# Performance work log

Measured on AMD Instinct MI355X. Metric: run time of the kernel, lower is better.

## Reference

```python
import jax, jax.numpy as jnp
import numpy as np


def setup_inputs() -> dict:
    key = jax.random.key(0)
    B, T, V, H, C = 128, 256, 128, 512, 128  # batch, seq_length, input_dim, num_hidden, num_classes
    ks = jax.random.split(key, 10)

    def xavier(k, shape):
        fan_in, fan_out = shape
        lim = jnp.sqrt(6.0 / (fan_in + fan_out)).astype(jnp.float32)
        return jax.random.uniform(k, shape, jnp.float32, -lim, lim)

    inp = {
        'x': jax.random.randint(ks[0], (B, T), 0, V, dtype=jnp.int32),
        'W_xg': xavier(ks[1], (V, H)), 'W_hg': xavier(ks[2], (H, H)),
        'W_xi': xavier(ks[3], (V, H)), 'W_hi': xavier(ks[4], (H, H)),
        'W_xf': xavier(ks[5], (V, H)), 'W_hf': xavier(ks[6], (H, H)),
        'W_xo': xavier(ks[7], (V, H)), 'W_ho': xavier(ks[8], (H, H)),
        'W_hp': xavier(ks[9], (H, C)),
        'b_g': jnp.zeros((H,), jnp.float32), 'b_i': jnp.zeros((H,), jnp.float32),
        'b_f': jnp.zeros((H,), jnp.float32), 'b_o': jnp.zeros((H,), jnp.float32),
        'b_p': jnp.zeros((C,), jnp.float32),
    }
    return inp


def reference(x, W_xg, W_hg, W_xi, W_hi, W_xf, W_hf, W_xo, W_ho, W_hp,
              b_g, b_i, b_f, b_o, b_p):
    B, T = x.shape
    H = W_hg.shape[0]
    # one-hot(x_t) @ W_x* == row-gather W_x*[x_t]; same math, no dense one-hot.
    xs = x[:, : T - 1].T  # [T-1, B] token ids; loop runs seq_length-1 steps

    def step(carry, idx):
        h, c = carry
        g = jnp.tanh(W_xg[idx] + h @ W_hg + b_g)
        i = jax.nn.sigmoid(W_xi[idx] + h @ W_hi + b_i)
        f = jax.nn.sigmoid(W_xf[idx] + h @ W_hf + b_f)
        o = jax.nn.sigmoid(W_xo[idx] + h @ W_ho + b_o)
        c = g * i + c * f
        h = jnp.tanh(c) * o
        return (h, c), None

    h0 = jnp.zeros((B, H), jnp.float32)
    c0 = jnp.zeros((B, H), jnp.float32)
    (h, _), _ = jax.lax.scan(step, (h0, c0), xs)
    return h @ W_hp + b_p
```

## Files before the change

kernel.cpp:

```cpp
#include <hip/hip_runtime.h>


typedef __attribute__((ext_vector_type(8))) short short8;
typedef __attribute__((ext_vector_type(4))) float f32x4;
typedef __attribute__((ext_vector_type(8))) unsigned int u32x8;
typedef __attribute__((ext_vector_type(16))) unsigned int u32x16;

#define NGROUPS 8
#define WGS_PER_GROUP 32
#define HDIM 512
#define TT 256
#define NSTEPS 255
#define CDIM 128
#define PGW 8192
#define PLANE_W 4096
#define TAGB_OFF 1024

__device__ unsigned int g_hbuf[4 * NGROUPS * PGW];
__device__ unsigned int g_sync[TAGB_OFF + NGROUPS * WGS_PER_GROUP * 16];

static __device__ __forceinline__ unsigned short f32_to_bf16(float f) {
  unsigned int u = __builtin_bit_cast(unsigned int, f);
  u += 0x7fffu + ((u >> 16) & 1u);
  return (unsigned short)(u >> 16);
}
static __device__ __forceinline__ float bf16_to_f32(unsigned short s) {
  unsigned int u = ((unsigned int)s) << 16;
  return __builtin_bit_cast(float, u);
}
static __device__ __forceinline__ float fast_sigmoid(float v) {
  return __builtin_amdgcn_rcpf(1.0f + __expf(-v));
}
static __device__ __forceinline__ float fast_tanh(float v) {
  return 1.0f - 2.0f * __builtin_amdgcn_rcpf(1.0f + __expf(2.0f * v));
}
static __device__ __forceinline__ const unsigned int* sgpr_ptr(const unsigned int* p) {
  const unsigned long long u = (unsigned long long)p;
  const unsigned int lo = __builtin_amdgcn_readfirstlane((unsigned int)u);
  const unsigned int hi = __builtin_amdgcn_readfirstlane((unsigned int)(u >> 32));
  return (const unsigned int*)(((unsigned long long)hi << 32) | (unsigned long long)lo);
}

static __device__ __forceinline__ unsigned int poll_min8(const unsigned int* p) {
  u32x8 A;
  asm volatile("s_dcache_inv\n\t"
               "s_load_dwordx8 %0, %1, 0x0\n\t"
               "s_waitcnt lgkmcnt(0)"
               : "=&s"(A) : "s"(p) : "memory");
  unsigned int m = A[0];
#pragma unroll
  for (int i = 1; i < 8; ++i) m = (A[i] < m) ? A[i] : m;
  return m;
}
static __device__ __forceinline__ unsigned int poll_min32(const unsigned int* p) {
  u32x16 A, B;
  asm volatile("s_dcache_inv\n\t"
               "s_load_dwordx16 %0, %1, 0x0\n\t"
               "s_waitcnt lgkmcnt(0)"
               : "=&s"(A) : "s"(p) : "memory");
  unsigned int m = A[0];
#pragma unroll
  for (int i = 1; i < 16; ++i) m = (A[i] < m) ? A[i] : m;
  asm volatile("s_load_dwordx16 %0, %1, 0x40\n\t"
               "s_waitcnt lgkmcnt(0)"
               : "=&s"(B) : "s"(p) : "memory");
#pragma unroll
  for (int i = 0; i < 16; ++i) m = (B[i] < m) ? B[i] : m;
  return m;
}

static __device__ __forceinline__ void wait_prod8(const unsigned int* tag8,
                                                  const unsigned int* tagBlane,
                                                  unsigned int tgt) {
  for (int spins = 0; spins < 4096; ++spins) {
    if (poll_min8(tag8) >= tgt) return;
  }
  for (;;) {
    const unsigned int v = __hip_atomic_load(tagBlane, __ATOMIC_RELAXED,
                                             __HIP_MEMORY_SCOPE_AGENT);
    if (__all((int)(v >= tgt))) return;
    __builtin_amdgcn_s_sleep(1);
  }
}
static __device__ __forceinline__ void wait_group32(const unsigned int* tagA,
                                                    const unsigned int* tagBlane,
                                                    unsigned int tgt) {
  for (int spins = 0; spins < 4096; ++spins) {
    if (poll_min32(tagA) >= tgt) return;
  }
  for (;;) {
    const unsigned int v = __hip_atomic_load(tagBlane, __ATOMIC_RELAXED,
                                             __HIP_MEMORY_SCOPE_AGENT);
    if (__all((int)(v >= tgt))) return;
    __builtin_amdgcn_s_sleep(1);
  }
}

__global__ __launch_bounds__(256, 1) void lstm_persistent(
    const int* __restrict__ x,
    const float* __restrict__ Wxg, const float* __restrict__ Whg,
    const float* __restrict__ Wxi, const float* __restrict__ Whi,
    const float* __restrict__ Wxf, const float* __restrict__ Whf,
    const float* __restrict__ Wxo, const float* __restrict__ Who,
    const float* __restrict__ Whp,
    const float* __restrict__ bg, const float* __restrict__ bi,
    const float* __restrict__ bf, const float* __restrict__ bo,
    const float* __restrict__ bp,
    float* __restrict__ out)
{
  const int bid = blockIdx.x;
  const int g = bid & 7;
  const int w = bid >> 3;
  const int tid = threadIdx.x;
  const int wave = tid >> 6;
  const int lane = tid & 63;
  const int lane15 = lane & 15;
  const int lanehi = lane >> 4;

  __shared__ __align__(16) float part[2][4][16][16][4];
  __shared__ int lds_x[16][TT];
  __shared__ unsigned int lds_ctr;

  if (tid == 0) lds_ctr = 0u;
  for (int i = tid; i < 16 * TT; i += 256)
    ((int*)lds_x)[i] = x[g * 16 * TT + i];

  const float* Whs[4] = {Whg, Whi, Whf, Who};
  const int bcol = (w << 4) + lane15;
  short8 wf[4][4][2];
#pragma unroll
  for (int gate = 0; gate < 4; ++gate) {
    const float* Wh = Whs[gate];
#pragma unroll
    for (int ksl = 0; ksl < 4; ++ksl) {
      const int ksg = (wave << 2) + ksl;
      short8 s0, s1;
#pragma unroll
      for (int e = 0; e < 8; ++e) {
        float v = Wh[(ksg * 32 + lanehi * 8 + e) * HDIM + bcol];
        unsigned short a = f32_to_bf16(v);
        unsigned short b = f32_to_bf16(v - bf16_to_f32(a));
        s0[e] = (short)a; s1[e] = (short)b;
      }
      wf[gate][ksl][0] = s0; wf[gate][ksl][1] = s1;
    }
  }
  __syncthreads();

  const int brow = tid >> 4;
  const int jl = tid & 15;
  const int j = (w << 4) + jl;
  const float bgv = bg[j], biv = bi[j], bfv = bf[j], bov = bo[j];
  const int woff32 = ((j >> 5) << 8) + ((((j >> 3) & 3) << 4) + brow) * 4 + ((j & 7) >> 1);
  const unsigned int voff = ((unsigned)wave << 12) + ((unsigned)lane << 4);

  const unsigned int* tagA = sgpr_ptr(g_sync + (g << 5));
  const unsigned int* tag8 = sgpr_ptr(g_sync + (g << 5) + (wave << 3));
  const unsigned int* tagBlane =
      g_sync + TAGB_OFF + ((unsigned)(g * 32 + (lane & 31)) << 4);
  unsigned int* myA = g_sync + (g << 5) + w;
  unsigned int* myB = g_sync + TAGB_OFF + ((unsigned)(g * 32 + w) << 4);

  float creg = 0.0f;

  for (int t = 0; t < NSTEPS; ++t) {
    const int idx = lds_x[brow][t];
    const float xgv = Wxg[idx * HDIM + j];
    const float xiv = Wxi[idx * HDIM + j];
    const float xfv = Wxf[idx * HDIM + j];
    const float xov = Wxo[idx * HDIM + j];

    f32x4 accA[4] = {{0.f,0.f,0.f,0.f},{0.f,0.f,0.f,0.f},
                     {0.f,0.f,0.f,0.f},{0.f,0.f,0.f,0.f}};
    f32x4 accB[4] = {{0.f,0.f,0.f,0.f},{0.f,0.f,0.f,0.f},
                     {0.f,0.f,0.f,0.f},{0.f,0.f,0.f,0.f}};
    if (t > 0) {
      wait_prod8(tag8, tagBlane, (unsigned int)t);
      const char* p0 = (const char*)(g_hbuf +
          ((size_t)((t & 3) * NGROUPS + g)) * PGW) + voff;
      short8 a0[4], a1[4];
#pragma unroll
      for (int ksl = 0; ksl < 4; ++ksl) {
        a0[ksl] = *(const short8*)(p0 + ksl * 1024);
        a1[ksl] = *(const short8*)(p0 + PLANE_W * 4 + ksl * 1024);
      }
#pragma unroll
      for (int ksl = 0; ksl < 2; ++ksl) {
#pragma unroll
        for (int gate = 0; gate < 4; ++gate) {
          accA[gate] = __builtin_amdgcn_mfma_f32_16x16x32_bf16(a0[ksl], wf[gate][ksl][0], accA[gate], 0, 0, 0);
          accA[gate] = __builtin_amdgcn_mfma_f32_16x16x32_bf16(a0[ksl], wf[gate][ksl][1], accA[gate], 0, 0, 0);
          accA[gate] = __builtin_amdgcn_mfma_f32_16x16x32_bf16(a1[ksl], wf[gate][ksl][0], accA[gate], 0, 0, 0);
        }
      }
#pragma unroll
      for (int ksl = 2; ksl < 4; ++ksl) {
#pragma unroll
        for (int gate = 0; gate < 4; ++gate) {
          accB[gate] = __builtin_amdgcn_mfma_f32_16x16x32_bf16(a0[ksl], wf[gate][ksl][0], accB[gate], 0, 0, 0);
          accB[gate] = __builtin_amdgcn_mfma_f32_16x16x32_bf16(a0[ksl], wf[gate][ksl][1], accB[gate], 0, 0, 0);
          accB[gate] = __builtin_amdgcn_mfma_f32_16x16x32_bf16(a1[ksl], wf[gate][ksl][0], accB[gate], 0, 0, 0);
        }
      }
    }
    {
      const int crow = lanehi << 2;
      const int pb = t & 1;
#pragma unroll
      for (int r = 0; r < 4; ++r) {
        f32x4 vr;
#pragma unroll
        for (int gate = 0; gate < 4; ++gate)
          vr[gate] = accA[gate][r] + accB[gate][r];
        *(f32x4*)&part[pb][wave][crow + r][lane15][0] = vr;
      }
    }
    __syncthreads();

    const int pb = t & 1;
    const f32x4 s0 = *(const f32x4*)&part[pb][0][brow][jl][0];
    const f32x4 s1 = *(const f32x4*)&part[pb][1][brow][jl][0];
    const f32x4 s2 = *(const f32x4*)&part[pb][2][brow][jl][0];
    const f32x4 s3 = *(const f32x4*)&part[pb][3][brow][jl][0];
    const f32x4 pre = s0 + s1 + s2 + s3;
    const float pg = pre[0] + xgv + bgv;
    const float pi = pre[1] + xiv + biv;
    const float pf = pre[2] + xfv + bfv;
    const float po = pre[3] + xov + bov;
    const float gv = fast_tanh(pg);
    const float iv = fast_sigmoid(pi);
    const float fv = fast_sigmoid(pf);
    const float ov = fast_sigmoid(po);
    creg = gv * iv + creg * fv;
    const float hv = fast_tanh(creg) * ov;

    const unsigned short h0 = f32_to_bf16(hv);
    const unsigned short h1 = f32_to_bf16(hv - bf16_to_f32(h0));
    const unsigned int pa = (unsigned int)h0 | ((unsigned int)h1 << 16);
    const unsigned int na = (unsigned int)__shfl_xor((int)pa, 1);
    if (!(jl & 1)) {
      unsigned int* dst0 = g_hbuf +
          ((size_t)(((t + 1) & 3) * NGROUPS + g)) * PGW;
      const unsigned int w0 = (pa & 0xffffu) | ((na & 0xffffu) << 16);
      const unsigned int w1 = (pa >> 16) | (na & 0xffff0000u);
      dst0[woff32] = w0;
      dst0[PLANE_W + woff32] = w1;
    }
    asm volatile("s_waitcnt vmcnt(0)" ::: "memory");
    if (lane == 0) {
      const unsigned int old = atomicAdd(&lds_ctr, 1u);
      if ((old & 3u) == 3u) {
        __hip_atomic_store(myA, (unsigned int)(t + 1), __ATOMIC_RELAXED,
                           __HIP_MEMORY_SCOPE_WORKGROUP);
        __hip_atomic_store(myB, (unsigned int)(t + 1), __ATOMIC_RELAXED,
                           __HIP_MEMORY_SCOPE_AGENT);
      }
    }
  }

  wait_group32(tagA, tagBlane, (unsigned int)NSTEPS);
  __syncthreads();
  {
    const unsigned int* src =
        g_hbuf + ((size_t)((NSTEPS & 3) * NGROUPS + g)) * PGW;
    const int bq = tid >> 4;
    const int q15 = tid & 15;
    const int cloc = q15 >> 2;
    const int ksl2 = q15 & 3;
    const int cc = (w << 2) + cloc;
    float sum = 0.0f;
    for (int k = ksl2 * 128; k < ksl2 * 128 + 128; k += 2) {
      const int pk = ((k >> 5) << 8) + ((((k >> 3) & 3) << 4) + bq) * 4 + ((k & 7) >> 1);
      const unsigned int w0 = src[pk];
      const unsigned int w1 = src[PLANE_W + pk];
      const float hk0 = bf16_to_f32((unsigned short)(w0 & 0xffffu)) +
                        bf16_to_f32((unsigned short)(w1 & 0xffffu));
      const float hk1 = bf16_to_f32((unsigned short)(w0 >> 16)) +
                        bf16_to_f32((unsigned short)(w1 >> 16));
      sum += hk0 * Whp[k * CDIM + cc] + hk1 * Whp[(k + 1) * CDIM + cc];
    }
    float* gb = &part[0][0][0][0][0];
    gb[tid] = sum;
    __syncthreads();
    if (ksl2 == 0) {
      const float res = gb[tid] + gb[tid + 1] + gb[tid + 2] + gb[tid + 3] + bp[cc];
      out[(g * 16 + bq) * CDIM + cc] = res;
    }
  }
}

extern "C" void kernel_launch(void* const* d_in, const int* in_sizes, int n_in,
                              void* d_out, int out_size, void* d_ws, size_t ws_size,
                              hipStream_t stream) {
  (void)in_sizes; (void)n_in; (void)out_size; (void)d_ws; (void)ws_size;
  const int* x = (const int*)d_in[0];
  const float* Wxg = (const float*)d_in[1];
  const float* Whg = (const float*)d_in[2];
  const float* Wxi = (const float*)d_in[3];
  const float* Whi = (const float*)d_in[4];
  const float* Wxf = (const float*)d_in[5];
  const float* Whf = (const float*)d_in[6];
  const float* Wxo = (const float*)d_in[7];
  const float* Who = (const float*)d_in[8];
  const float* Whp = (const float*)d_in[9];
  const float* bg = (const float*)d_in[10];
  const float* bi = (const float*)d_in[11];
  const float* bf = (const float*)d_in[12];
  const float* bo = (const float*)d_in[13];
  const float* bp = (const float*)d_in[14];
  float* out = (float*)d_out;

  void* sync_dev = nullptr;
  hipGetSymbolAddress(&sync_dev, HIP_SYMBOL(g_sync));
  hipMemsetAsync(sync_dev, 0,
                 sizeof(unsigned int) * (TAGB_OFF + NGROUPS * WGS_PER_GROUP * 16),
                 stream);

  lstm_persistent<<<dim3(256), dim3(256), 0, stream>>>(
      x, Wxg, Whg, Wxi, Whi, Wxf, Whf, Wxo, Who, Whp,
      bg, bi, bf, bo, bp, out);
}
```

Baseline: 418.1 us.

## Use per-wave readiness flags and consume h chunks as producers finish

Each wave now publishes its own step flag, replacing the per-workgroup flag that was raised after an LDS atomic counter reached four waves. Consumers poll 32 per-wave flags split into four K-chunks and run the MFMAs for each chunk as soon as its producers are ready, rather than waiting for all producers first. This overlaps part of the recurrent matmul with the inter-workgroup wait on the critical serial path. In exchange there are more flag stores, a larger polling set, and separate accumulators per chunk, which raises register pressure.

```diff
diff --git a/kernel.cpp b/kernel.cpp
--- a/kernel.cpp
+++ b/kernel.cpp
@@ -4,7 +4,6 @@
 typedef __attribute__((ext_vector_type(8))) short short8;
 typedef __attribute__((ext_vector_type(4))) float f32x4;
 typedef __attribute__((ext_vector_type(8))) unsigned int u32x8;
-typedef __attribute__((ext_vector_type(16))) unsigned int u32x16;
 
 #define NGROUPS 8
 #define WGS_PER_GROUP 32
@@ -17,7 +16,7 @@
 #define TAGB_OFF 1024
 
 __device__ unsigned int g_hbuf[4 * NGROUPS * PGW];
-__device__ unsigned int g_sync[TAGB_OFF + NGROUPS * WGS_PER_GROUP * 16];
+__device__ unsigned int g_sync[TAGB_OFF + 1024 * 16];
 
 static __device__ __forceinline__ unsigned short f32_to_bf16(float f) {
   unsigned int u = __builtin_bit_cast(unsigned int, f);
@@ -40,60 +39,14 @@
   const unsigned int hi = __builtin_amdgcn_readfirstlane((unsigned int)(u >> 32));
   return (const unsigned int*)(((unsigned long long)hi << 32) | (unsigned long long)lo);
 }
-
-static __device__ __forceinline__ unsigned int poll_min8(const unsigned int* p) {
-  u32x8 A;
-  asm volatile("s_dcache_inv\n\t"
-               "s_load_dwordx8 %0, %1, 0x0\n\t"
-               "s_waitcnt lgkmcnt(0)"
-               : "=&s"(A) : "s"(p) : "memory");
+static __device__ __forceinline__ unsigned int vmin8(u32x8 A) {
   unsigned int m = A[0];
 #pragma unroll
   for (int i = 1; i < 8; ++i) m = (A[i] < m) ? A[i] : m;
   return m;
 }
-static __device__ __forceinline__ unsigned int poll_min32(const unsigned int* p) {
-  u32x16 A, B;
-  asm volatile("s_dcache_inv\n\t"
-               "s_load_dwordx16 %0, %1, 0x0\n\t"
-               "s_waitcnt lgkmcnt(0)"
-               : "=&s"(A) : "s"(p) : "memory");
-  unsigned int m = A[0];
-#pragma unroll
-  for (int i = 1; i < 16; ++i) m = (A[i] < m) ? A[i] : m;
-  asm volatile("s_load_dwordx16 %0, %1, 0x40\n\t"
-               "s_waitcnt lgkmcnt(0)"
-               : "=&s"(B) : "s"(p) : "memory");
-#pragma unroll
-  for (int i = 0; i < 16; ++i) m = (B[i] < m) ? B[i] : m;
-  return m;
-}
-
-static __device__ __forceinline__ void wait_prod8(const unsigned int* tag8,
-                                                  const unsigned int* tagBlane,
-                                                  unsigned int tgt) {
-  for (int spins = 0; spins < 4096; ++spins) {
-    if (poll_min8(tag8) >= tgt) return;
-  }
-  for (;;) {
-    const unsigned int v = __hip_atomic_load(tagBlane, __ATOMIC_RELAXED,
-                                             __HIP_MEMORY_SCOPE_AGENT);
-    if (__all((int)(v >= tgt))) return;
-    __builtin_amdgcn_s_sleep(1);
-  }
-}
-static __device__ __forceinline__ void wait_group32(const unsigned int* tagA,
-                                                    const unsigned int* tagBlane,
-                                                    unsigned int tgt) {
-  for (int spins = 0; spins < 4096; ++spins) {
-    if (poll_min32(tagA) >= tgt) return;
-  }
-  for (;;) {
-    const unsigned int v = __hip_atomic_load(tagBlane, __ATOMIC_RELAXED,
-                                             __HIP_MEMORY_SCOPE_AGENT);
-    if (__all((int)(v >= tgt))) return;
-    __builtin_amdgcn_s_sleep(1);
-  }
+static __device__ __forceinline__ unsigned int ag_ld(const unsigned int* p) {
+  return __hip_atomic_load(p, __ATOMIC_RELAXED, __HIP_MEMORY_SCOPE_AGENT);
 }
 
 __global__ __launch_bounds__(256, 1) void lstm_persistent(
@@ -119,9 +72,7 @@
 
   __shared__ __align__(16) float part[2][4][16][16][4];
   __shared__ int lds_x[16][TT];
-  __shared__ unsigned int lds_ctr;
-
-  if (tid == 0) lds_ctr = 0u;
+
   for (int i = tid; i < 16 * TT; i += 256)
     ((int*)lds_x)[i] = x[g * 16 * TT + i];
 
@@ -154,12 +105,11 @@
   const int woff32 = ((j >> 5) << 8) + ((((j >> 3) & 3) << 4) + brow) * 4 + ((j & 7) >> 1);
   const unsigned int voff = ((unsigned)wave << 12) + ((unsigned)lane << 4);
 
-  const unsigned int* tagA = sgpr_ptr(g_sync + (g << 5));
-  const unsigned int* tag8 = sgpr_ptr(g_sync + (g << 5) + (wave << 3));
-  const unsigned int* tagBlane =
-      g_sync + TAGB_OFF + ((unsigned)(g * 32 + (lane & 31)) << 4);
-  unsigned int* myA = g_sync + (g << 5) + w;
-  unsigned int* myB = g_sync + TAGB_OFF + ((unsigned)(g * 32 + w) << 4);
+  const unsigned int* tf = sgpr_ptr(g_sync + g * 128 + 32 * wave);
+  unsigned int* myF = g_sync + g * 128 + w * 4 + wave;
+  unsigned int* myB = g_sync + TAGB_OFF + (unsigned)(g * 128 + w * 4 + wave) * 16;
+  const unsigned int* fbl = g_sync + TAGB_OFF +
+      (unsigned)(g * 128 + 32 * wave + (lane & 31)) * 16;
 
   float creg = 0.0f;
 
@@ -170,39 +120,61 @@
     const float xfv = Wxf[idx * HDIM + j];
     const float xov = Wxo[idx * HDIM + j];
 
-    f32x4 accA[4] = {{0.f,0.f,0.f,0.f},{0.f,0.f,0.f,0.f},
-                     {0.f,0.f,0.f,0.f},{0.f,0.f,0.f,0.f}};
-    f32x4 accB[4] = {{0.f,0.f,0.f,0.f},{0.f,0.f,0.f,0.f},
-                     {0.f,0.f,0.f,0.f},{0.f,0.f,0.f,0.f}};
+    f32x4 acc[4][4];
+#pragma unroll
+    for (int k2 = 0; k2 < 4; ++k2)
+#pragma unroll
+      for (int gg = 0; gg < 4; ++gg) acc[k2][gg] = f32x4{0.f, 0.f, 0.f, 0.f};
+
     if (t > 0) {
-      wait_prod8(tag8, tagBlane, (unsigned int)t);
+      const unsigned int ut = (unsigned int)t;
       const char* p0 = (const char*)(g_hbuf +
           ((size_t)((t & 3) * NGROUPS + g)) * PGW) + voff;
-      short8 a0[4], a1[4];
-#pragma unroll
-      for (int ksl = 0; ksl < 4; ++ksl) {
-        a0[ksl] = *(const short8*)(p0 + ksl * 1024);
-        a1[ksl] = *(const short8*)(p0 + PLANE_W * 4 + ksl * 1024);
-      }
-#pragma unroll
-      for (int ksl = 0; ksl < 2; ++ksl) {
-#pragma unroll
-        for (int gate = 0; gate < 4; ++gate) {
-          accA[gate] = __builtin_amdgcn_mfma_f32_16x16x32_bf16(a0[ksl], wf[gate][ksl][0], accA[gate], 0, 0, 0);
-          accA[gate] = __builtin_amdgcn_mfma_f32_16x16x32_bf16(a0[ksl], wf[gate][ksl][1], accA[gate], 0, 0, 0);
-          accA[gate] = __builtin_amdgcn_mfma_f32_16x16x32_bf16(a1[ksl], wf[gate][ksl][0], accA[gate], 0, 0, 0);
+
+#define CHUNK(K) do {                                                         \
+      asm volatile("" ::: "memory");       \
+      const short8 a0_ = *(const short8*)(p0 + (K) * 1024);                   \
+      const short8 a1_ = *(const short8*)(p0 + 16384 + (K) * 1024);           \
+      _Pragma("unroll")                                                       \
+      for (int gg = 0; gg < 4; ++gg) {                                        \
+        acc[K][gg] = __builtin_amdgcn_mfma_f32_16x16x32_bf16(a0_, wf[gg][K][0], acc[K][gg], 0, 0, 0); \
+        acc[K][gg] = __builtin_amdgcn_mfma_f32_16x16x32_bf16(a0_, wf[gg][K][1], acc[K][gg], 0, 0, 0); \
+        acc[K][gg] = __builtin_amdgcn_mfma_f32_16x16x32_bf16(a1_, wf[gg][K][0], acc[K][gg], 0, 0, 0); \
+      } } while (0)
+
+      unsigned int done = 0;
+      int guard = 0;
+      while (done != 0xFu) {
+        u32x8 A0, A1, A2, A3;
+        asm volatile("s_dcache_inv\n\t"
+                     "s_load_dwordx8 %0, %4, 0\n\t"
+                     "s_load_dwordx8 %1, %4, 32\n\t"
+                     "s_load_dwordx8 %2, %4, 64\n\t"
+                     "s_load_dwordx8 %3, %4, 96\n\t"
+                     "s_waitcnt lgkmcnt(0)"
+                     : "=&s"(A0), "=&s"(A1), "=&s"(A2), "=&s"(A3)
+                     : "s"(tf) : "memory");
+        if (!(done & 1u) && vmin8(A0) >= ut) { CHUNK(0); done |= 1u; }
+        if (!(done & 2u) && vmin8(A1) >= ut) { CHUNK(1); done |= 2u; }
+        if (!(done & 4u) && vmin8(A2) >= ut) { CHUNK(2); done |= 4u; }
+        if (!(done & 8u) && vmin8(A3) >= ut) { CHUNK(3); done |= 8u; }
+        if (++guard > 8192 && done != 0xFu) {
+          for (;;) {
+            const unsigned int v = ag_ld(fbl);
+            if (__all((int)(v >= ut))) break;
+            __builtin_amdgcn_s_sleep(1);
+          }
+          asm volatile("" ::: "memory");
+          if (!(done & 1u)) CHUNK(0);
+          if (!(done & 2u)) CHUNK(1);
+          if (!(done & 4u)) CHUNK(2);
+          if (!(done & 8u)) CHUNK(3);
+          done = 0xFu;
         }
       }
-#pragma unroll
-      for (int ksl = 2; ksl < 4; ++ksl) {
-#pragma unroll
-        for (int gate = 0; gate < 4; ++gate) {
-          accB[gate] = __builtin_amdgcn_mfma_f32_16x16x32_bf16(a0[ksl], wf[gate][ksl][0], accB[gate], 0, 0, 0);
-          accB[gate] = __builtin_amdgcn_mfma_f32_16x16x32_bf16(a0[ksl], wf[gate][ksl][1], accB[gate], 0, 0, 0);
-          accB[gate] = __builtin_amdgcn_mfma_f32_16x16x32_bf16(a1[ksl], wf[gate][ksl][0], accB[gate], 0, 0, 0);
-        }
-      }
-    }
+#undef CHUNK
+    }
+
     {
       const int crow = lanehi << 2;
       const int pb = t & 1;
@@ -210,8 +182,8 @@
       for (int r = 0; r < 4; ++r) {
         f32x4 vr;
 #pragma unroll
-        for (int gate = 0; gate < 4; ++gate)
-          vr[gate] = accA[gate][r] + accB[gate][r];
+        for (int gg = 0; gg < 4; ++gg)
+          vr[gg] = (acc[0][gg][r] + acc[1][gg][r]) + (acc[2][gg][r] + acc[3][gg][r]);
         *(f32x4*)&part[pb][wave][crow + r][lane15][0] = vr;
       }
     }
@@ -248,17 +220,24 @@
     }
     asm volatile("s_waitcnt vmcnt(0)" ::: "memory");
     if (lane == 0) {
-      const unsigned int old = atomicAdd(&lds_ctr, 1u);
-      if ((old & 3u) == 3u) {
-        __hip_atomic_store(myA, (unsigned int)(t + 1), __ATOMIC_RELAXED,
-                           __HIP_MEMORY_SCOPE_WORKGROUP);
-        __hip_atomic_store(myB, (unsigned int)(t + 1), __ATOMIC_RELAXED,
-                           __HIP_MEMORY_SCOPE_AGENT);
-      }
+      __hip_atomic_store(myF, (unsigned int)(t + 1), __ATOMIC_RELAXED,
+                         __HIP_MEMORY_SCOPE_WORKGROUP);
+      __hip_atomic_store(myB, (unsigned int)(t + 1), __ATOMIC_RELAXED,
+                         __HIP_MEMORY_SCOPE_AGENT);
     }
   }
 
-  wait_group32(tagA, tagBlane, (unsigned int)NSTEPS);
+  {
+    const unsigned int* b0 = g_sync + TAGB_OFF + (unsigned)(g * 128 + lane) * 16;
+    const unsigned int* b1 = g_sync + TAGB_OFF + (unsigned)(g * 128 + 64 + lane) * 16;
+    for (;;) {
+      const unsigned int va = ag_ld(b0);
+      const unsigned int vb = ag_ld(b1);
+      if (__all((int)(va >= (unsigned)NSTEPS && vb >= (unsigned)NSTEPS))) break;
+      __builtin_amdgcn_s_sleep(1);
+    }
+  }
+  asm volatile("" ::: "memory");
   __syncthreads();
   {
     const unsigned int* src =
@@ -312,8 +291,7 @@
 
   void* sync_dev = nullptr;
   hipGetSymbolAddress(&sync_dev, HIP_SYMBOL(g_sync));
-  hipMemsetAsync(sync_dev, 0,
-                 sizeof(unsigned int) * (TAGB_OFF + NGROUPS * WGS_PER_GROUP * 16),
+  hipMemsetAsync(sync_dev, 0, sizeof(unsigned int) * (TAGB_OFF + 1024 * 16),
                  stream);
 
   lstm_persistent<<<dim3(256), dim3(256), 0, stream>>>(
```

New measurement: 549.2 us. 1.31x slower.

## Halve workgroups per group, doubling columns and K-split waves per block

Applied to the files above, without the earlier changes.

Restructures the persistent LSTM from 256 blocks of 256 threads to 128 blocks of 512 threads. Each block now owns 32 hidden columns and splits K over 8 waves, so each wave polls only 2 producer flags instead of 8. Per-group barrier fan-in drops from 32 to 16 producers. The cost is a deeper LDS reduction across 8 partials, and token ids are now read from global memory each step instead of being staged in LDS.

```diff
diff --git a/kernel.cpp b/kernel.cpp
--- a/kernel.cpp
+++ b/kernel.cpp
@@ -3,21 +3,21 @@
 
 typedef __attribute__((ext_vector_type(8))) short short8;
 typedef __attribute__((ext_vector_type(4))) float f32x4;
-typedef __attribute__((ext_vector_type(8))) unsigned int u32x8;
+typedef __attribute__((ext_vector_type(2))) unsigned int u32x2;
 typedef __attribute__((ext_vector_type(16))) unsigned int u32x16;
 
 #define NGROUPS 8
-#define WGS_PER_GROUP 32
+#define WPG 16
 #define HDIM 512
 #define TT 256
 #define NSTEPS 255
 #define CDIM 128
 #define PGW 8192
 #define PLANE_W 4096
-#define TAGB_OFF 1024
+#define TAGB_OFF 256
 
 __device__ unsigned int g_hbuf[4 * NGROUPS * PGW];
-__device__ unsigned int g_sync[TAGB_OFF + NGROUPS * WGS_PER_GROUP * 16];
+__device__ unsigned int g_sync[TAGB_OFF + NGROUPS * WPG * 16];
 
 static __device__ __forceinline__ unsigned short f32_to_bf16(float f) {
   unsigned int u = __builtin_bit_cast(unsigned int, f);
@@ -40,20 +40,20 @@
   const unsigned int hi = __builtin_amdgcn_readfirstlane((unsigned int)(u >> 32));
   return (const unsigned int*)(((unsigned long long)hi << 32) | (unsigned long long)lo);
 }
-
-static __device__ __forceinline__ unsigned int poll_min8(const unsigned int* p) {
-  u32x8 A;
+static __device__ __forceinline__ unsigned int ag_ld(const unsigned int* p) {
+  return __hip_atomic_load(p, __ATOMIC_RELAXED, __HIP_MEMORY_SCOPE_AGENT);
+}
+
+static __device__ __forceinline__ unsigned int poll_min2(const unsigned int* p) {
+  u32x2 A;
   asm volatile("s_dcache_inv\n\t"
-               "s_load_dwordx8 %0, %1, 0x0\n\t"
+               "s_load_dwordx2 %0, %1, 0x0\n\t"
                "s_waitcnt lgkmcnt(0)"
                : "=&s"(A) : "s"(p) : "memory");
-  unsigned int m = A[0];
-#pragma unroll
-  for (int i = 1; i < 8; ++i) m = (A[i] < m) ? A[i] : m;
-  return m;
-}
-static __device__ __forceinline__ unsigned int poll_min32(const unsigned int* p) {
-  u32x16 A, B;
+  return (A[0] < A[1]) ? A[0] : A[1];
+}
+static __device__ __forceinline__ unsigned int poll_min16(const unsigned int* p) {
+  u32x16 A;
   asm volatile("s_dcache_inv\n\t"
                "s_load_dwordx16 %0, %1, 0x0\n\t"
                "s_waitcnt lgkmcnt(0)"
@@ -61,42 +61,34 @@
   unsigned int m = A[0];
 #pragma unroll
   for (int i = 1; i < 16; ++i) m = (A[i] < m) ? A[i] : m;
-  asm volatile("s_load_dwordx16 %0, %1, 0x40\n\t"
-               "s_waitcnt lgkmcnt(0)"
-               : "=&s"(B) : "s"(p) : "memory");
-#pragma unroll
-  for (int i = 0; i < 16; ++i) m = (B[i] < m) ? B[i] : m;
   return m;
 }
-
-static __device__ __forceinline__ void wait_prod8(const unsigned int* tag8,
-                                                  const unsigned int* tagBlane,
+static __device__ __forceinline__ void wait_prod2(const unsigned int* tf,
+                                                  const unsigned int* fbl,
                                                   unsigned int tgt) {
-  for (int spins = 0; spins < 4096; ++spins) {
-    if (poll_min8(tag8) >= tgt) return;
+  for (int spins = 0; spins < 8192; ++spins) {
+    if (poll_min2(tf) >= tgt) return;
   }
   for (;;) {
-    const unsigned int v = __hip_atomic_load(tagBlane, __ATOMIC_RELAXED,
-                                             __HIP_MEMORY_SCOPE_AGENT);
+    const unsigned int v = ag_ld(fbl);
     if (__all((int)(v >= tgt))) return;
     __builtin_amdgcn_s_sleep(1);
   }
 }
-static __device__ __forceinline__ void wait_group32(const unsigned int* tagA,
-                                                    const unsigned int* tagBlane,
+static __device__ __forceinline__ void wait_group16(const unsigned int* tagA,
+                                                    const unsigned int* fbl,
                                                     unsigned int tgt) {
-  for (int spins = 0; spins < 4096; ++spins) {
-    if (poll_min32(tagA) >= tgt) return;
+  for (int spins = 0; spins < 8192; ++spins) {
+    if (poll_min16(tagA) >= tgt) return;
   }
   for (;;) {
-    const unsigned int v = __hip_atomic_load(tagBlane, __ATOMIC_RELAXED,
-                                             __HIP_MEMORY_SCOPE_AGENT);
+    const unsigned int v = ag_ld(fbl);
     if (__all((int)(v >= tgt))) return;
     __builtin_amdgcn_s_sleep(1);
   }
 }
 
-__global__ __launch_bounds__(256, 1) void lstm_persistent(
+__global__ __launch_bounds__(512, 2) void lstm_persistent(
     const int* __restrict__ x,
     const float* __restrict__ Wxg, const float* __restrict__ Whg,
     const float* __restrict__ Wxi, const float* __restrict__ Whi,
@@ -112,94 +104,92 @@
   const int g = bid & 7;
   const int w = bid >> 3;
   const int tid = threadIdx.x;
-  const int wave = tid >> 6;
+  const int kq = tid >> 6;
   const int lane = tid & 63;
   const int lane15 = lane & 15;
   const int lanehi = lane >> 4;
 
-  __shared__ __align__(16) float part[2][4][16][16][4];
-  __shared__ int lds_x[16][TT];
+  __shared__ __align__(16) float part[2][8][16][32][4];
   __shared__ unsigned int lds_ctr;
 
   if (tid == 0) lds_ctr = 0u;
-  for (int i = tid; i < 16 * TT; i += 256)
-    ((int*)lds_x)[i] = x[g * 16 * TT + i];
 
   const float* Whs[4] = {Whg, Whi, Whf, Who};
-  const int bcol = (w << 4) + lane15;
-  short8 wf[4][4][2];
-#pragma unroll
-  for (int gate = 0; gate < 4; ++gate) {
-    const float* Wh = Whs[gate];
-#pragma unroll
-    for (int ksl = 0; ksl < 4; ++ksl) {
-      const int ksg = (wave << 2) + ksl;
-      short8 s0, s1;
-#pragma unroll
-      for (int e = 0; e < 8; ++e) {
-        float v = Wh[(ksg * 32 + lanehi * 8 + e) * HDIM + bcol];
-        unsigned short a = f32_to_bf16(v);
-        unsigned short b = f32_to_bf16(v - bf16_to_f32(a));
-        s0[e] = (short)a; s1[e] = (short)b;
+  short8 wf[2][2][4][2];
+#pragma unroll
+  for (int ch = 0; ch < 2; ++ch) {
+    const int bcol = (w << 5) + (ch << 4) + lane15;
+#pragma unroll
+    for (int c = 0; c < 2; ++c) {
+      const int ks = (kq << 1) + c;
+#pragma unroll
+      for (int gate = 0; gate < 4; ++gate) {
+        const float* Wh = Whs[gate];
+        short8 s0, s1;
+#pragma unroll
+        for (int e = 0; e < 8; ++e) {
+          float v = Wh[(ks * 32 + lanehi * 8 + e) * HDIM + bcol];
+          unsigned short a = f32_to_bf16(v);
+          unsigned short b = f32_to_bf16(v - bf16_to_f32(a));
+          s0[e] = (short)a; s1[e] = (short)b;
+        }
+        wf[ch][c][gate][0] = s0; wf[ch][c][gate][1] = s1;
       }
-      wf[gate][ksl][0] = s0; wf[gate][ksl][1] = s1;
     }
   }
   __syncthreads();
 
-  const int brow = tid >> 4;
-  const int jl = tid & 15;
-  const int j = (w << 4) + jl;
+  const int brow = tid >> 5;
+  const int cl = tid & 31;
+  const int j = (w << 5) + cl;
+  const int rowg = g * 16 + brow;
   const float bgv = bg[j], biv = bi[j], bfv = bf[j], bov = bo[j];
   const int woff32 = ((j >> 5) << 8) + ((((j >> 3) & 3) << 4) + brow) * 4 + ((j & 7) >> 1);
-  const unsigned int voff = ((unsigned)wave << 12) + ((unsigned)lane << 4);
-
-  const unsigned int* tagA = sgpr_ptr(g_sync + (g << 5));
-  const unsigned int* tag8 = sgpr_ptr(g_sync + (g << 5) + (wave << 3));
-  const unsigned int* tagBlane =
-      g_sync + TAGB_OFF + ((unsigned)(g * 32 + (lane & 31)) << 4);
-  unsigned int* myA = g_sync + (g << 5) + w;
-  unsigned int* myB = g_sync + TAGB_OFF + ((unsigned)(g * 32 + w) << 4);
+
+  const unsigned int* tagA = sgpr_ptr(g_sync + (g << 4));
+  const unsigned int* tf = sgpr_ptr(g_sync + (g << 4) + (kq << 1));
+  unsigned int* myA = g_sync + (g << 4) + w;
+  unsigned int* myB = g_sync + TAGB_OFF + ((unsigned)(g * WPG + w) << 4);
+  const unsigned int* fbl = g_sync + TAGB_OFF +
+      ((unsigned)(g * WPG + (kq << 1) + (lane & 1)) << 4);
+  const unsigned int* fblE = g_sync + TAGB_OFF +
+      ((unsigned)(g * WPG + (lane & 15)) << 4);
 
   float creg = 0.0f;
 
   for (int t = 0; t < NSTEPS; ++t) {
-    const int idx = lds_x[brow][t];
+    const int idx = x[rowg * TT + t];
     const float xgv = Wxg[idx * HDIM + j];
     const float xiv = Wxi[idx * HDIM + j];
     const float xfv = Wxf[idx * HDIM + j];
     const float xov = Wxo[idx * HDIM + j];
 
-    f32x4 accA[4] = {{0.f,0.f,0.f,0.f},{0.f,0.f,0.f,0.f},
-                     {0.f,0.f,0.f,0.f},{0.f,0.f,0.f,0.f}};
-    f32x4 accB[4] = {{0.f,0.f,0.f,0.f},{0.f,0.f,0.f,0.f},
-                     {0.f,0.f,0.f,0.f},{0.f,0.f,0.f,0.f}};
+    f32x4 acc[2][4];
+#pragma unroll
+    for (int ch = 0; ch < 2; ++ch)
+#pragma unroll
+      for (int gate = 0; gate < 4; ++gate) acc[ch][gate] = f32x4{0.f,0.f,0.f,0.f};
+
     if (t > 0) {
-      wait_prod8(tag8, tagBlane, (unsigned int)t);
+      wait_prod2(tf, fbl, (unsigned int)t);
       const char* p0 = (const char*)(g_hbuf +
-          ((size_t)((t & 3) * NGROUPS + g)) * PGW) + voff;
-      short8 a0[4], a1[4];
-#pragma unroll
-      for (int ksl = 0; ksl < 4; ++ksl) {
-        a0[ksl] = *(const short8*)(p0 + ksl * 1024);
-        a1[ksl] = *(const short8*)(p0 + PLANE_W * 4 + ksl * 1024);
+          ((size_t)((t & 3) * NGROUPS + g)) * PGW) + (kq << 11) + (lane << 4);
+      short8 a0[2], a1[2];
+#pragma unroll
+      for (int c = 0; c < 2; ++c) {
+        a0[c] = *(const short8*)(p0 + c * 1024);
+        a1[c] = *(const short8*)(p0 + PLANE_W * 4 + c * 1024);
       }
 #pragma unroll
-      for (int ksl = 0; ksl < 2; ++ksl) {
-#pragma unroll
-        for (int gate = 0; gate < 4; ++gate) {
-          accA[gate] = __builtin_amdgcn_mfma_f32_16x16x32_bf16(a0[ksl], wf[gate][ksl][0], accA[gate], 0, 0, 0);
-          accA[gate] = __builtin_amdgcn_mfma_f32_16x16x32_bf16(a0[ksl], wf[gate][ksl][1], accA[gate], 0, 0, 0);
-          accA[gate] = __builtin_amdgcn_mfma_f32_16x16x32_bf16(a1[ksl], wf[gate][ksl][0], accA[gate], 0, 0, 0);
-        }
-      }
-#pragma unroll
-      for (int ksl = 2; ksl < 4; ++ksl) {
-#pragma unroll
-        for (int gate = 0; gate < 4; ++gate) {
-          accB[gate] = __builtin_amdgcn_mfma_f32_16x16x32_bf16(a0[ksl], wf[gate][ksl][0], accB[gate], 0, 0, 0);
-          accB[gate] = __builtin_amdgcn_mfma_f32_16x16x32_bf16(a0[ksl], wf[gate][ksl][1], accB[gate], 0, 0, 0);
-          accB[gate] = __builtin_amdgcn_mfma_f32_16x16x32_bf16(a1[ksl], wf[gate][ksl][0], accB[gate], 0, 0, 0);
+      for (int c = 0; c < 2; ++c) {
+#pragma unroll
+        for (int ch = 0; ch < 2; ++ch) {
+#pragma unroll
+          for (int gate = 0; gate < 4; ++gate) {
+            acc[ch][gate] = __builtin_amdgcn_mfma_f32_16x16x32_bf16(a0[c], wf[ch][c][gate][0], acc[ch][gate], 0, 0, 0);
+            acc[ch][gate] = __builtin_amdgcn_mfma_f32_16x16x32_bf16(a0[c], wf[ch][c][gate][1], acc[ch][gate], 0, 0, 0);
+            acc[ch][gate] = __builtin_amdgcn_mfma_f32_16x16x32_bf16(a1[c], wf[ch][c][gate][0], acc[ch][gate], 0, 0, 0);
+          }
         }
       }
     }
@@ -207,22 +197,22 @@
       const int crow = lanehi << 2;
       const int pb = t & 1;
 #pragma unroll
-      for (int r = 0; r < 4; ++r) {
-        f32x4 vr;
-#pragma unroll
-        for (int gate = 0; gate < 4; ++gate)
-          vr[gate] = accA[gate][r] + accB[gate][r];
-        *(f32x4*)&part[pb][wave][crow + r][lane15][0] = vr;
-      }
+      for (int ch = 0; ch < 2; ++ch)
+#pragma unroll
+        for (int r = 0; r < 4; ++r) {
+          f32x4 vr;
+#pragma unroll
+          for (int gate = 0; gate < 4; ++gate) vr[gate] = acc[ch][gate][r];
+          *(f32x4*)&part[pb][kq][crow + r][(ch << 4) + lane15][0] = vr;
+        }
     }
     __syncthreads();
 
     const int pb = t & 1;
-    const f32x4 s0 = *(const f32x4*)&part[pb][0][brow][jl][0];
-    const f32x4 s1 = *(const f32x4*)&part[pb][1][brow][jl][0];
-    const f32x4 s2 = *(const f32x4*)&part[pb][2][brow][jl][0];
-    const f32x4 s3 = *(const f32x4*)&part[pb][3][brow][jl][0];
-    const f32x4 pre = s0 + s1 + s2 + s3;
+    f32x4 pre = *(const f32x4*)&part[pb][0][brow][cl][0];
+#pragma unroll
+    for (int q = 1; q < 8; ++q)
+      pre += *(const f32x4*)&part[pb][q][brow][cl][0];
     const float pg = pre[0] + xgv + bgv;
     const float pi = pre[1] + xiv + biv;
     const float pf = pre[2] + xfv + bfv;
@@ -238,7 +228,7 @@
     const unsigned short h1 = f32_to_bf16(hv - bf16_to_f32(h0));
     const unsigned int pa = (unsigned int)h0 | ((unsigned int)h1 << 16);
     const unsigned int na = (unsigned int)__shfl_xor((int)pa, 1);
-    if (!(jl & 1)) {
+    if (!(cl & 1)) {
       unsigned int* dst0 = g_hbuf +
           ((size_t)(((t + 1) & 3) * NGROUPS + g)) * PGW;
       const unsigned int w0 = (pa & 0xffffu) | ((na & 0xffffu) << 16);
@@ -249,7 +239,7 @@
     asm volatile("s_waitcnt vmcnt(0)" ::: "memory");
     if (lane == 0) {
       const unsigned int old = atomicAdd(&lds_ctr, 1u);
-      if ((old & 3u) == 3u) {
+      if ((old & 7u) == 7u) {
         __hip_atomic_store(myA, (unsigned int)(t + 1), __ATOMIC_RELAXED,
                            __HIP_MEMORY_SCOPE_WORKGROUP);
         __hip_atomic_store(myB, (unsigned int)(t + 1), __ATOMIC_RELAXED,
@@ -258,16 +248,16 @@
     }
   }
 
-  wait_group32(tagA, tagBlane, (unsigned int)NSTEPS);
+  wait_group16(tagA, fblE, (unsigned int)NSTEPS);
   __syncthreads();
   {
     const unsigned int* src =
         g_hbuf + ((size_t)((NSTEPS & 3) * NGROUPS + g)) * PGW;
-    const int bq = tid >> 4;
-    const int q15 = tid & 15;
-    const int cloc = q15 >> 2;
-    const int ksl2 = q15 & 3;
-    const int cc = (w << 2) + cloc;
+    const int bq = tid >> 5;
+    const int q31 = tid & 31;
+    const int cloc = q31 >> 2;
+    const int ksl2 = q31 & 3;
+    const int cc = (w << 3) + cloc;
     float sum = 0.0f;
     for (int k = ksl2 * 128; k < ksl2 * 128 + 128; k += 2) {
       const int pk = ((k >> 5) << 8) + ((((k >> 3) & 3) << 4) + bq) * 4 + ((k & 7) >> 1);
@@ -313,10 +303,10 @@
   void* sync_dev = nullptr;
   hipGetSymbolAddress(&sync_dev, HIP_SYMBOL(g_sync));
   hipMemsetAsync(sync_dev, 0,
-                 sizeof(unsigned int) * (TAGB_OFF + NGROUPS * WGS_PER_GROUP * 16),
+                 sizeof(unsigned int) * (TAGB_OFF + NGROUPS * WPG * 16),
                  stream);
 
-  lstm_persistent<<<dim3(256), dim3(256), 0, stream>>>(
+  lstm_persistent<<<dim3(128), dim3(512), 0, stream>>>(
       x, Wxg, Whg, Wxi, Whi, Wxf, Whf, Wxo, Who, Whp,
       bg, bi, bf, bo, bp, out);
 }
```

Measured after the change: 555.8 us. +32.9%, slower.
